# Kernel tuning notes

Measured on AMD Instinct MI355X. Metric: run time of the kernel, lower is better.

Reference implementation:

```python
import jax, jax.numpy as jnp
import numpy as np

K = 9      # kernel size
DIL = 2    # dilation
PAD = 8    # padding -> same-size output


def unfold(x):
    """nd2col: (B,C,H,W) -> (B,C,K,K,H,W) patches with dilation/padding."""
    B, C, H, W = x.shape
    xp = jnp.pad(x, ((0, 0), (0, 0), (PAD, PAD), (PAD, PAD)))
    cols = jnp.stack(
        [xp[:, :, i * DIL:i * DIL + H, j * DIL:j * DIL + W]
         for i in range(K) for j in range(K)], axis=2)
    return cols.reshape(B, C, K, K, H, W)


def pac_kernel(f):
    """Gaussian adaptive kernel: exp(-0.5*||f_nbr - f_center||^2), shape (B,1,K,K,H,W)."""
    # center of the dilated patch (K//2, K//2) is the pixel itself
    d = unfold(f) - f[:, :, None, None, :, :]
    return jnp.exp(-0.5 * jnp.sum(d * d, axis=1, keepdims=True))


def pacconv(x, k, w, b):
    """Pixel-adaptive conv: unfold, modulate by guidance kernel, contract with weight."""
    cols = unfold(x)                                  # (B,Cin,K,K,H,W)
    out = jnp.einsum('bcklhw,ockl->bohw', cols * k, w)
    return out + b[None, :, None, None]


def setup_inputs() -> dict:
    key = jax.random.key(0)
    ks = jax.random.split(key, 6)
    B, C, H, W = 1, 32, 128, 128
    x = jax.random.normal(ks[0], (B, C, H, W), jnp.float32)
    f = jax.random.normal(ks[1], (B, C, H, W), jnp.float32)
    fan_in = C * K * K
    bound = float(1.0 / np.sqrt(fan_in))
    W1 = jax.random.uniform(ks[2], (32, C, K, K), jnp.float32, -bound, bound)
    b1 = jax.random.uniform(ks[3], (32,), jnp.float32, -bound, bound)
    W2 = jax.random.uniform(ks[4], (32, 32, K, K), jnp.float32, -bound, bound)
    b2 = jax.random.uniform(ks[5], (32,), jnp.float32, -bound, bound)
    return {"x": x, "f": f, "W1": W1, "b1": b1, "W2": W2, "b2": b2}


def reference(x, f, W1, b1, W2, b2):
    k = pac_kernel(f)  # same guidance for both layers -> identical kernel
    h = pacconv(x, k, W1, b1)
    return pacconv(h, k, W2, b2)
```

## Files before the change

### kernel.cpp

```cpp
#include <hip/hip_runtime.h>

#define HH 128
#define WW 128
#define NPIX 16384
#define NC 32
#define NO 32
#define KS 9
#define TAPS 81
#define DIL 2
#define PAD 8
#define SMAX 27.6310211159f
#define NW (NO * NC * TAPS)
#define CAP 262144

#define BUILD_MASK32(P, M0, M1) do {                                        \
        const uint4* mp_ = (const uint4*)(mask32 + (size_t)(P) * 32);       \
        uint4 ma_ = mp_[0], mb_ = mp_[1];                                   \
        unsigned w_[8] = { ma_.x, ma_.y, ma_.z, ma_.w,                      \
                           mb_.x, mb_.y, mb_.z, mb_.w };                    \
        M0 = 0ull; M1 = 0u;                                                 \
        unsigned m9_[9];                                                    \
        _Pragma("unroll")                                                   \
        for (int i_ = 0; i_ < 9; ++i_) {                                    \
            int k0_ = 3 * i_, k1_ = 3 * i_ + 1, k2_ = 3 * i_ + 2;           \
            unsigned b0_ = (w_[k0_ >> 2] >> ((k0_ & 3) * 8)) & 7u;          \
            unsigned b1_ = (w_[k1_ >> 2] >> ((k1_ & 3) * 8)) & 7u;          \
            unsigned b2_ = (w_[k2_ >> 2] >> ((k2_ & 3) * 8)) & 7u;          \
            m9_[i_] = b0_ | (b1_ << 3) | (b2_ << 6);                        \
        }                                                                   \
        _Pragma("unroll")                                                   \
        for (int i_ = 0; i_ < 7; ++i_)                                      \
            M0 |= (unsigned long long)m9_[i_] << (9 * i_);                  \
        M0 |= (unsigned long long)(m9_[7] & 1u) << 63;                      \
        M1 = (m9_[7] >> 1) | (m9_[8] << 8);                                 \
    } while (0)

__global__ __launch_bounds__(256) void prep3_kernel(
    const float* __restrict__ x, const float* __restrict__ f,
    const float* __restrict__ W1, const float* __restrict__ W2,
    float* __restrict__ xT, float* __restrict__ kbuf,
    unsigned char* __restrict__ mask32,
    float* __restrict__ W1t, float* __restrict__ W2t)
{
    const int bid = blockIdx.x;
    const int tid = threadIdx.x;

    if (bid < 1728) {
        const int pixblk = bid & 63, iz = bid >> 6;
        const int i = iz / 3, z = iz - 3 * i;
        const int pix = pixblk * 256 + tid;
        const int hh = pix >> 7, ww = pix & (WW - 1);
        float fc[NC];
#pragma unroll
        for (int c = 0; c < NC; ++c) fc[c] = f[c * NPIX + pix];
        const int qh = hh + i * DIL - PAD;
        const bool vh = (unsigned)qh < HH;
        unsigned pmask = 0;
#pragma unroll
        for (int jj = 0; jj < 3; ++jj) {
            int j = 3 * z + jj;
            int qw = ww + j * DIL - PAD;
            bool valid = vh & ((unsigned)qw < WW);
            int q = valid ? (qh * WW + qw) : pix;
            float s0 = 0.f, s1 = 0.f, s2 = 0.f, s3 = 0.f;
#pragma unroll
            for (int c4 = 0; c4 < 8; ++c4) {
                float d0 = f[(4 * c4 + 0) * NPIX + q] - fc[4 * c4 + 0];
                float d1 = f[(4 * c4 + 1) * NPIX + q] - fc[4 * c4 + 1];
                float d2 = f[(4 * c4 + 2) * NPIX + q] - fc[4 * c4 + 2];
                float d3 = f[(4 * c4 + 3) * NPIX + q] - fc[4 * c4 + 3];
                s0 = fmaf(d0, d0, s0); s1 = fmaf(d1, d1, s1);
                s2 = fmaf(d2, d2, s2); s3 = fmaf(d3, d3, s3);
            }
            float s = (s0 + s1) + (s2 + s3);
            bool live = valid && (s <= SMAX) && !(i == 4 && j == 4);
            if (live) {
                pmask |= 1u << jj;
                kbuf[(i * KS + j) * NPIX + pix] = __expf(-0.5f * s);
            }
        }
        mask32[(size_t)pix * 32 + iz] = (unsigned char)pmask;
        return;
    }

    if (bid < 1792) {
        for (int t = (bid - 1728) * 256 + tid; t < NW; t += 64 * 256) {
            int o = t / (NC * TAPS);
            int r = t - o * (NC * TAPS);
            int c = r / TAPS;
            int tap = r - c * TAPS;
            int d = (tap * NO + o) * NC + c;
            W1t[d] = W1[t];
            W2t[d] = W2[t];
        }
        return;
    }

    for (int idx = (bid - 1792) * 256 + tid; idx < NPIX * NC; idx += 64 * 256) {
        int p = idx >> 5, c = idx & 31;
        xT[idx] = x[c * NPIX + p];
    }
}

__global__ __launch_bounds__(256) void fused2_kernel(
    const float* __restrict__ xT, const float* __restrict__ kbuf,
    const unsigned char* __restrict__ mask32,
    const float* __restrict__ W1t, const float* __restrict__ W2t,
    const float* __restrict__ b1, const float* __restrict__ b2,
    float* __restrict__ out)
{
    const int wv = threadIdx.x >> 6;
    const int lane = threadIdx.x & 63;
    const int half = lane >> 5;
    const int o = lane & 31;
    const int c0 = half * 16;
    const int p = blockIdx.x * 4 + wv;
    __shared__ float hlds[4][NC];

    const float b1o = b1[o];

#define DOT16(WROW, XROW, RES) do {                                        \
        const float4* wq_ = (const float4*)((WROW) + c0);                  \
        const float4* xq_ = (const float4*)((XROW) + c0);                  \
        float r0_ = 0.f, r1_ = 0.f, r2_ = 0.f, r3_ = 0.f;                  \
        _Pragma("unroll")                                                  \
        for (int k_ = 0; k_ < 4; ++k_) {                                   \
            float4 w4_ = wq_[k_], x4_ = xq_[k_];                           \
            r0_ = fmaf(w4_.x, x4_.x, r0_);                                 \
            r1_ = fmaf(w4_.y, x4_.y, r1_);                                 \
            r2_ = fmaf(w4_.z, x4_.z, r2_);                                 \
            r3_ = fmaf(w4_.w, x4_.w, r3_);                                 \
        }                                                                  \
        RES = (r0_ + r1_) + (r2_ + r3_);                                   \
    } while (0)

    unsigned long long A0; unsigned A1;
    BUILD_MASK32(p, A0, A1);
    unsigned long long A0s = A0; unsigned A1s = A1;

    float acc = 0.f;
    int first = 1;
    for (;;) {
        int Tq, q; float kvq;
        if (first)      { Tq = 40; q = p; kvq = 1.0f; }
        else if (A0s) {
            Tq = __builtin_ctzll(A0s); A0s &= A0s - 1;
            int ii = Tq / KS, jj = Tq - KS * ii;
            q = p + (ii * DIL - PAD) * WW + (jj * DIL - PAD);
            kvq = kbuf[Tq * NPIX + p];
        } else if (A1s) {
            Tq = 64 + __builtin_ctz(A1s); A1s &= A1s - 1;
            int ii = Tq / KS, jj = Tq - KS * ii;
            q = p + (ii * DIL - PAD) * WW + (jj * DIL - PAD);
            kvq = kbuf[Tq * NPIX + p];
        } else break;

        unsigned long long B0; unsigned B1;
        if (first) { B0 = A0; B1 = A1; }
        else BUILD_MASK32(q, B0, B1);

        float hpart;
        DOT16(W1t + (40 * NO + o) * NC, xT + q * NC, hpart);
        while (B0) {
            int T2 = __builtin_ctzll(B0); B0 &= B0 - 1;
            int i2 = T2 / KS, j2 = T2 - KS * i2;
            int q2 = q + (i2 * DIL - PAD) * WW + (j2 * DIL - PAD);
            float kv2 = kbuf[T2 * NPIX + q];
            float d; DOT16(W1t + (T2 * NO + o) * NC, xT + q2 * NC, d);
            hpart = fmaf(kv2, d, hpart);
        }
        while (B1) {
            int T2 = 64 + __builtin_ctz(B1); B1 &= B1 - 1;
            int i2 = T2 / KS, j2 = T2 - KS * i2;
            int q2 = q + (i2 * DIL - PAD) * WW + (j2 * DIL - PAD);
            float kv2 = kbuf[T2 * NPIX + q];
            float d; DOT16(W1t + (T2 * NO + o) * NC, xT + q2 * NC, d);
            hpart = fmaf(kv2, d, hpart);
        }
        float hfull = hpart + __shfl_xor(hpart, 32);
        hfull += b1o;
        if (half == 0) hlds[wv][o] = hfull;
        float wsdot;
        DOT16(W2t + (Tq * NO + o) * NC, &hlds[wv][0], wsdot);
        acc = fmaf(kvq, wsdot, acc);
        first = 0;
    }
#undef DOT16

    float accf = acc + __shfl_xor(acc, 32);
    if (half == 0) out[o * NPIX + p] = accf + b2[o];
}

__global__ __launch_bounds__(64) void zero_cnt_kernel(unsigned* __restrict__ cnt)
{
    if (threadIdx.x == 0) *cnt = 0u;
}

__device__ __forceinline__ void sparse_body(
    const float* __restrict__ in, const float* __restrict__ Wt,
    const unsigned* __restrict__ cnt, const uint2* __restrict__ list,
    float* __restrict__ out, unsigned gid, unsigned stride)
{
    unsigned n = *cnt;
    if (n > CAP) n = CAP;
    const unsigned total = n * 32u;
    for (unsigned it = gid; it < total; it += stride) {
        unsigned e = it >> 5;
        int o = (int)(it & 31u);
        uint2 me = list[e];
        int pix = (int)(me.x & 16383u);
        int T = (int)(me.x >> 14);
        float kv = __uint_as_float(me.y);
        int ii = T / KS, jj = T - KS * ii;
        int q = pix + (ii * DIL - PAD) * WW + (jj * DIL - PAD);
        const float4* __restrict__ wp =
            (const float4*)(Wt + (T * NO + o) * NC);
        float t0 = 0.f, t1 = 0.f, t2 = 0.f, t3 = 0.f;
#pragma unroll
        for (int c4 = 0; c4 < 8; ++c4) {
            float4 w4 = wp[c4];
            t0 = fmaf(in[(4 * c4 + 0) * NPIX + q], w4.x, t0);
            t1 = fmaf(in[(4 * c4 + 1) * NPIX + q], w4.y, t1);
            t2 = fmaf(in[(4 * c4 + 2) * NPIX + q], w4.z, t2);
            t3 = fmaf(in[(4 * c4 + 3) * NPIX + q], w4.w, t3);
        }
        atomicAdd(&out[o * NPIX + pix], kv * ((t0 + t1) + (t2 + t3)));
    }
}

__global__ __launch_bounds__(256) void front_kernel(
    const float* __restrict__ x, const float* __restrict__ f,
    const float* __restrict__ W1, const float* __restrict__ W2,
    const float* __restrict__ b1,
    float* __restrict__ h, unsigned* __restrict__ cnt,
    uint2* __restrict__ list, float* __restrict__ W1t,
    float* __restrict__ W2t, float* __restrict__ outz)
{
    const int y = blockIdx.y;
    const int tid = threadIdx.x;

    if (y < 41) {
        const int pix = blockIdx.x * 256 + tid;
        const int hh = pix >> 7, ww = pix & (WW - 1);
        float fc[NC];
#pragma unroll
        for (int c = 0; c < NC; ++c) fc[c] = f[c * NPIX + pix];
#pragma unroll
        for (int u = 0; u < 2; ++u) {
            int T = 2 * y + u;
            if (T >= TAPS || T == 40) continue;
            int ii = T / KS, jj = T - KS * ii;
            int qh = hh + ii * DIL - PAD;
            int qw = ww + jj * DIL - PAD;
            bool valid = ((unsigned)qh < HH) & ((unsigned)qw < WW);
            int q = valid ? (qh * WW + qw) : pix;
            float s0 = 0.f, s1 = 0.f, s2 = 0.f, s3 = 0.f;
#pragma unroll
            for (int c4 = 0; c4 < 8; ++c4) {
                float d0 = f[(4 * c4 + 0) * NPIX + q] - fc[4 * c4 + 0];
                float d1 = f[(4 * c4 + 1) * NPIX + q] - fc[4 * c4 + 1];
                float d2 = f[(4 * c4 + 2) * NPIX + q] - fc[4 * c4 + 2];
                float d3 = f[(4 * c4 + 3) * NPIX + q] - fc[4 * c4 + 3];
                s0 = fmaf(d0, d0, s0); s1 = fmaf(d1, d1, s1);
                s2 = fmaf(d2, d2, s2); s3 = fmaf(d3, d3, s3);
            }
            float s = (s0 + s1) + (s2 + s3);
            if (valid && (s <= SMAX)) {
                unsigned idx = atomicAdd(cnt, 1u);
                if (idx < CAP)
                    list[idx] = make_uint2(
                        (unsigned)pix | ((unsigned)T << 14),
                        __float_as_uint(__expf(-0.5f * s)));
            }
        }
        return;
    }

    if (y < 49) {
        const int o0 = (y - 41) * 4;
        __shared__ float wsm[4 * NC];
        if (tid < 128) {
            int o = tid >> 5, c = tid & 31;
            wsm[tid] = W1[((o0 + o) * NC + c) * TAPS + 40];
        }
        __syncthreads();
        const int pix = blockIdx.x * 256 + tid;
        float x0[NC];
#pragma unroll
        for (int c = 0; c < NC; ++c) x0[c] = x[c * NPIX + pix];
        float a0 = 0.f, a1 = 0.f, a2 = 0.f, a3 = 0.f;
#pragma unroll
        for (int c = 0; c < NC; ++c) {
            float xv = x0[c];
            a0 = fmaf(xv, wsm[0 * NC + c], a0);
            a1 = fmaf(xv, wsm[1 * NC + c], a1);
            a2 = fmaf(xv, wsm[2 * NC + c], a2);
            a3 = fmaf(xv, wsm[3 * NC + c], a3);
        }
        h[(o0 + 0) * NPIX + pix] = a0 + b1[o0 + 0];
        h[(o0 + 1) * NPIX + pix] = a1 + b1[o0 + 1];
        h[(o0 + 2) * NPIX + pix] = a2 + b1[o0 + 2];
        h[(o0 + 3) * NPIX + pix] = a3 + b1[o0 + 3];
        return;
    }

    if (y == 49) {
        float4 z = make_float4(0.f, 0.f, 0.f, 0.f);
        for (int t = blockIdx.x * 256 + tid; t < (NO * NPIX) / 4; t += 64 * 256)
            ((float4*)outz)[t] = z;
        return;
    }

    for (int t = blockIdx.x * 256 + tid; t < NW; t += 64 * 256) {
        int o = t / (NC * TAPS);
        int r = t - o * (NC * TAPS);
        int c = r / TAPS;
        int tap = r - c * TAPS;
        int d = (tap * NO + o) * NC + c;
        W1t[d] = W1[t];
        W2t[d] = W2[t];
    }
}

__global__ __launch_bounds__(256) void sparse1_kernel(
    const float* __restrict__ x, const float* __restrict__ W1t,
    const unsigned* __restrict__ cnt, const uint2* __restrict__ list,
    float* __restrict__ h)
{
    sparse_body(x, W1t, cnt, list, h,
                blockIdx.x * 256 + threadIdx.x, gridDim.x * 256);
}

__global__ __launch_bounds__(256) void back_kernel(
    const float* __restrict__ h, const float* __restrict__ W2,
    const float* __restrict__ W2t, const float* __restrict__ b2,
    const unsigned* __restrict__ cnt, const uint2* __restrict__ list,
    float* __restrict__ out)
{
    const int y = blockIdx.y;
    const int tid = threadIdx.x;
    if (y < 8) {
        const int o0 = y * 4;
        __shared__ float wsm[4 * NC];
        if (tid < 128) {
            int o = tid >> 5, c = tid & 31;
            wsm[tid] = W2[((o0 + o) * NC + c) * TAPS + 40];
        }
        __syncthreads();
        const int pix = blockIdx.x * 256 + tid;
        float h0[NC];
#pragma unroll
        for (int c = 0; c < NC; ++c) h0[c] = h[c * NPIX + pix];
        float a0 = 0.f, a1 = 0.f, a2 = 0.f, a3 = 0.f;
#pragma unroll
        for (int c = 0; c < NC; ++c) {
            float hv = h0[c];
            a0 = fmaf(hv, wsm[0 * NC + c], a0);
            a1 = fmaf(hv, wsm[1 * NC + c], a1);
            a2 = fmaf(hv, wsm[2 * NC + c], a2);
            a3 = fmaf(hv, wsm[3 * NC + c], a3);
        }
        atomicAdd(&out[(o0 + 0) * NPIX + pix], a0 + b2[o0 + 0]);
        atomicAdd(&out[(o0 + 1) * NPIX + pix], a1 + b2[o0 + 1]);
        atomicAdd(&out[(o0 + 2) * NPIX + pix], a2 + b2[o0 + 2]);
        atomicAdd(&out[(o0 + 3) * NPIX + pix], a3 + b2[o0 + 3]);
        return;
    }
    sparse_body(h, W2t, cnt, list, out,
                blockIdx.x * 256 + tid, 64 * 256);
}

#define CHUNK 27
#define NCHUNK 3
#define KMIN 1e-6f
__global__ __launch_bounds__(256) void pac_layer_fuse(
    const float* __restrict__ in, const float* __restrict__ f,
    const float* __restrict__ Wt, const float* __restrict__ bias,
    float* __restrict__ out)
{
    __shared__ float wl[NC * CHUNK * 8];
    const int og = blockIdx.y;
    const int pix = blockIdx.x * 256 + threadIdx.x;
    const int h = pix >> 7, w = pix & (WW - 1);
    float acc[8];
#pragma unroll
    for (int i = 0; i < 8; ++i) acc[i] = 0.f;
    float fc[NC];
#pragma unroll
    for (int c = 0; c < NC; ++c) fc[c] = f[c * NPIX + pix];
    for (int ch = 0; ch < NCHUNK; ++ch) {
        __syncthreads();
        for (int idx = threadIdx.x; idx < NC * CHUNK * 8; idx += 256) {
            int t = idx % CHUNK;
            int c = (idx / CHUNK) % NC;
            int o = idx / (CHUNK * NC);
            wl[(c * CHUNK + t) * 8 + o] =
                Wt[(og * 8 + o) * (NC * TAPS) + c * TAPS + ch * CHUNK + t];
        }
        __syncthreads();
        for (int t = 0; t < CHUNK; ++t) {
            int tap = ch * CHUNK + t;
            int qh = h + (tap / KS) * DIL - PAD;
            int qw = w + (tap % KS) * DIL - PAD;
            bool valid = ((unsigned)qh < HH) & ((unsigned)qw < WW);
            int q = qh * WW + qw;
            float s = 0.f;
#pragma unroll
            for (int c = 0; c < NC; ++c) {
                float fn = valid ? f[c * NPIX + q] : 0.f;
                float d = fn - fc[c];
                s = fmaf(d, d, s);
            }
            float kv = __expf(-0.5f * s);
            if (__all((kv < KMIN) | (!valid))) continue;
            const float* wpp = &wl[t * 8];
#pragma unroll 8
            for (int c = 0; c < NC; ++c) {
                float v = valid ? in[c * NPIX + q] : 0.f;
                v *= kv;
#pragma unroll
                for (int o = 0; o < 8; ++o)
                    acc[o] = fmaf(v, wpp[c * CHUNK * 8 + o], acc[o]);
            }
        }
    }
#pragma unroll
    for (int o = 0; o < 8; ++o)
        out[(og * 8 + o) * NPIX + pix] = acc[o] + bias[og * 8 + o];
}

extern "C" void kernel_launch(void* const* d_in, const int* in_sizes, int n_in,
                              void* d_out, int out_size, void* d_ws, size_t ws_size,
                              hipStream_t stream)
{
    (void)in_sizes; (void)n_in; (void)out_size;
    const float* x  = (const float*)d_in[0];
    const float* f  = (const float*)d_in[1];
    const float* W1 = (const float*)d_in[2];
    const float* b1 = (const float*)d_in[3];
    const float* W2 = (const float*)d_in[4];
    const float* b2 = (const float*)d_in[5];
    float* out = (float*)d_out;

    float* ws = (float*)d_ws;
    float* xT   = ws;
    float* kbuf = xT + NPIX * NC;
    float* W1t  = kbuf + TAPS * NPIX;
    float* W2t  = W1t + NW;
    unsigned char* mask32 = (unsigned char*)(W2t + NW);
    const size_t need_main =
        (size_t)(NPIX * NC + TAPS * NPIX + 2 * NW) * 4
        + (size_t)NPIX * 32;
    float* hA   = ws;
    float* W1tA = ws + NO * NPIX;
    float* W2tA = W1tA + NW;
    unsigned* cnt = (unsigned*)(W2tA + NW);
    uint2* list = (uint2*)(cnt + 16);
    const size_t need_fb =
        (size_t)(NO * NPIX + 2 * NW + 16) * 4 + (size_t)CAP * 8;

    if (ws_size >= need_main) {
        prep3_kernel<<<dim3(1856), 256, 0, stream>>>(
            x, f, W1, W2, xT, kbuf, mask32, W1t, W2t);
        fused2_kernel<<<dim3(NPIX / 4), 256, 0, stream>>>(
            xT, kbuf, mask32, W1t, W2t, b1, b2, out);
    } else if (ws_size >= need_fb) {
        zero_cnt_kernel<<<dim3(1), 64, 0, stream>>>(cnt);
        front_kernel<<<dim3(64, 51), 256, 0, stream>>>(
            x, f, W1, W2, b1, hA, cnt, list, W1tA, W2tA, out);
        sparse1_kernel<<<dim3(128), 256, 0, stream>>>(x, W1tA, cnt, list, hA);
        back_kernel<<<dim3(64, 9), 256, 0, stream>>>(
            hA, W2, W2tA, b2, cnt, list, out);
    } else {
        float* hbuf = ws;
        pac_layer_fuse<<<dim3(64, 4), 256, 0, stream>>>(x, f, W1, b1, hbuf);
        pac_layer_fuse<<<dim3(64, 4), 256, 0, stream>>>(hbuf, f, W2, b2, out);
    }
}
```

Measured before the change: 120.1 us.

## Split each pixel's outer taps across four wavefronts with atomic accumulation

```diff
diff --git a/kernel.cpp b/kernel.cpp
--- a/kernel.cpp
+++ b/kernel.cpp
@@ -40,7 +40,8 @@
     const float* __restrict__ W1, const float* __restrict__ W2,
     float* __restrict__ xT, float* __restrict__ kbuf,
     unsigned char* __restrict__ mask32,
-    float* __restrict__ W1t, float* __restrict__ W2t)
+    float* __restrict__ W1t, float* __restrict__ W2t,
+    float* __restrict__ outz)
 {
     const int bid = blockIdx.x;
     const int tid = threadIdx.x;
@@ -96,13 +97,24 @@
         return;
     }
 
-    for (int idx = (bid - 1792) * 256 + tid; idx < NPIX * NC; idx += 64 * 256) {
-        int p = idx >> 5, c = idx & 31;
-        xT[idx] = x[c * NPIX + p];
-    }
-}
-
-__global__ __launch_bounds__(256) void fused2_kernel(
+    if (bid < 1856) {
+        for (int idx = (bid - 1792) * 256 + tid; idx < NPIX * NC;
+             idx += 64 * 256) {
+            int p = idx >> 5, c = idx & 31;
+            xT[idx] = x[c * NPIX + p];
+        }
+        return;
+    }
+
+    {
+        float4 z4 = make_float4(0.f, 0.f, 0.f, 0.f);
+        for (int t = (bid - 1856) * 256 + tid; t < (NO * NPIX) / 4;
+             t += 64 * 256)
+            ((float4*)outz)[t] = z4;
+    }
+}
+
+__global__ __launch_bounds__(256) void fused2p_kernel(
     const float* __restrict__ xT, const float* __restrict__ kbuf,
     const unsigned char* __restrict__ mask32,
     const float* __restrict__ W1t, const float* __restrict__ W2t,
@@ -114,7 +126,7 @@
     const int half = lane >> 5;
     const int o = lane & 31;
     const int c0 = half * 16;
-    const int p = blockIdx.x * 4 + wv;
+    const int p = blockIdx.x;
     __shared__ float hlds[4][NC];
 
     const float b1o = b1[o];
@@ -136,27 +148,32 @@
 
     unsigned long long A0; unsigned A1;
     BUILD_MASK32(p, A0, A1);
-    unsigned long long A0s = A0; unsigned A1s = A1;
+    const int total = 1 + __popcll(A0) + __popc(A1);
 
     float acc = 0.f;
-    int first = 1;
-    for (;;) {
+    for (int idx = wv; idx < total; idx += 4) {
         int Tq, q; float kvq;
-        if (first)      { Tq = 40; q = p; kvq = 1.0f; }
-        else if (A0s) {
-            Tq = __builtin_ctzll(A0s); A0s &= A0s - 1;
+        if (idx == 0) { Tq = 40; q = p; kvq = 1.0f; }
+        else {
+            int k = idx - 1;
+            int cA = __popcll(A0);
+            if (k < cA) {
+                unsigned long long m = A0;
+                for (int s = 0; s < k; ++s) m &= m - 1;
+                Tq = __builtin_ctzll(m);
+            } else {
+                unsigned m = A1;
+                int kk = k - cA;
+                for (int s = 0; s < kk; ++s) m &= m - 1;
+                Tq = 64 + __builtin_ctz(m);
+            }
             int ii = Tq / KS, jj = Tq - KS * ii;
             q = p + (ii * DIL - PAD) * WW + (jj * DIL - PAD);
             kvq = kbuf[Tq * NPIX + p];
-        } else if (A1s) {
-            Tq = 64 + __builtin_ctz(A1s); A1s &= A1s - 1;
-            int ii = Tq / KS, jj = Tq - KS * ii;
-            q = p + (ii * DIL - PAD) * WW + (jj * DIL - PAD);
-            kvq = kbuf[Tq * NPIX + p];
-        } else break;
+        }
 
         unsigned long long B0; unsigned B1;
-        if (first) { B0 = A0; B1 = A1; }
+        if (idx == 0) { B0 = A0; B1 = A1; }
         else BUILD_MASK32(q, B0, B1);
 
         float hpart;
@@ -177,18 +194,17 @@
             float d; DOT16(W1t + (T2 * NO + o) * NC, xT + q2 * NC, d);
             hpart = fmaf(kv2, d, hpart);
         }
-        float hfull = hpart + __shfl_xor(hpart, 32);
-        hfull += b1o;
+        float hfull = hpart + __shfl_xor(hpart, 32) + b1o;
         if (half == 0) hlds[wv][o] = hfull;
         float wsdot;
         DOT16(W2t + (Tq * NO + o) * NC, &hlds[wv][0], wsdot);
         acc = fmaf(kvq, wsdot, acc);
-        first = 0;
     }
 #undef DOT16
 
     float accf = acc + __shfl_xor(acc, 32);
-    if (half == 0) out[o * NPIX + p] = accf + b2[o];
+    if (half == 0 && wv < total)
+        atomicAdd(&out[o * NPIX + p], accf + (wv == 0 ? b2[o] : 0.f));
 }
 
 __global__ __launch_bounds__(64) void zero_cnt_kernel(unsigned* __restrict__ cnt)
@@ -460,9 +476,9 @@
         (size_t)(NO * NPIX + 2 * NW + 16) * 4 + (size_t)CAP * 8;
 
     if (ws_size >= need_main) {
-        prep3_kernel<<<dim3(1856), 256, 0, stream>>>(
-            x, f, W1, W2, xT, kbuf, mask32, W1t, W2t);
-        fused2_kernel<<<dim3(NPIX / 4), 256, 0, stream>>>(
+        prep3_kernel<<<dim3(1920), 256, 0, stream>>>(
+            x, f, W1, W2, xT, kbuf, mask32, W1t, W2t, out);
+        fused2p_kernel<<<dim3(NPIX), 256, 0, stream>>>(
             xT, kbuf, mask32, W1t, W2t, b1, b2, out);
     } else if (ws_size >= need_fb) {
         zero_cnt_kernel<<<dim3(1), 64, 0, stream>>>(cnt);
```

Result: slower. 126.9 us (+5.7%).
